# Kernel optimization log

Hardware: AMD Instinct MI355X
Metric: run time of the kernel (lower is better)

The kernel has to match this reference:

```python
import jax, jax.numpy as jnp
import numpy as np

G, N, DEG = 64, 2048, 8          # graphs, nodes/graph, avg degree
NTOT = G * N                      # 131072 nodes
E = NTOT * DEG                    # 1048576 edges
K = int(np.ceil(0.2 * N))         # 410 nodes kept per graph (SAGPooling ratio=0.2)
NK = G * K                        # 26240 pooled nodes
H, C = 3, 20                      # GAT heads, per-head channels
NEG_BIG = jnp.float32(-1e30)


def gcn(x, src, dst, W, b, n):
    """PyG GCNConv: x' = D^-1/2 (A+I) D^-1/2 x W + b (edge weight 1)."""
    h = x @ W
    deg = jax.ops.segment_sum(jnp.ones(src.shape[0], x.dtype), dst, num_segments=n) + 1.0
    dinv = jax.lax.rsqrt(deg)
    coef = dinv[src] * dinv[dst]                    # [E]
    agg = jax.ops.segment_sum(h[src] * coef[:, None], dst, num_segments=n)
    agg = agg + h * (dinv * dinv)[:, None]          # self loops
    return agg + b


def setup_inputs() -> dict:
    key = jax.random.key(0)
    ks = jax.random.split(key, 16)
    # edges constrained within each graph: per-graph local indices + offsets
    off = jnp.repeat(jnp.arange(G, dtype=jnp.int32) * N, N * DEG)   # [E]
    src = jax.random.randint(ks[0], (E,), 0, N, dtype=jnp.int32) + off
    dst = jax.random.randint(ks[1], (E,), 0, N, dtype=jnp.int32) + off
    batch = jnp.repeat(jnp.arange(G, dtype=jnp.int32), N)           # [NTOT]
    x = jax.random.normal(ks[2], (NTOT, 5), jnp.float32)
    s = 0.1
    return {
        "x": x, "src": src, "dst": dst, "batch": batch,
        "W1": jax.random.normal(ks[3], (5, 10)) * s,   "b1": jnp.zeros((10,)),
        "Ws": jax.random.normal(ks[4], (10, 1)) * s,   "bs": jnp.zeros((1,)),
        "Wg": jax.random.normal(ks[5], (10, H * C)) * s,
        "a_src": jax.random.normal(ks[6], (H, C)) * s,
        "a_dst": jax.random.normal(ks[7], (H, C)) * s,
        "bg": jnp.zeros((H * C,)),
        "Wf1": jax.random.normal(ks[8], (60, 30)) * s, "bf1": jnp.zeros((30,)),
        "Wf2": jax.random.normal(ks[9], (30, 3)) * s,  "bf2": jnp.zeros((3,)),
    }


def reference(x, src, dst, batch, W1, b1, Ws, bs, Wg, a_src, a_dst, bg, Wf1, bf1, Wf2, bf2):
    n = x.shape[0]
    # GCNConv(5,10)
    x1 = gcn(x, src, dst, W1, b1, n)                              # [NTOT,10]
    # SAGPooling: GCN scorer, top-k per graph, gate by tanh(score)
    score = gcn(x1, src, dst, Ws, bs, n)[:, 0]                    # [NTOT]
    _, topi = jax.lax.top_k(score.reshape(G, N), K)               # [G,K]
    perm = (topi + (jnp.arange(G) * N)[:, None]).reshape(-1)      # [NK] global ids
    xp = x1[perm] * jnp.tanh(score[perm])[:, None]                # [NK,10]
    # remap edges; drop (mask) edges touching removed nodes (filter_adj)
    new_idx = jnp.full((n,), -1, jnp.int32).at[perm].set(jnp.arange(NK, dtype=jnp.int32))
    s2, d2 = new_idx[src], new_idx[dst]
    emask = (s2 >= 0) & (d2 >= 0)
    s2 = jnp.where(emask, s2, 0)
    d2 = jnp.where(emask, d2, 0)
    # GATConv(10, 20, heads=3) with self loops
    h = (xp @ Wg).reshape(NK, H, C)
    al_s = jnp.sum(h * a_src, -1)                                 # [NK,H]
    al_d = jnp.sum(h * a_dst, -1)
    loop = jnp.arange(NK, dtype=jnp.int32)
    sa = jnp.concatenate([s2, loop])
    da = jnp.concatenate([d2, loop])
    ma = jnp.concatenate([emask, jnp.ones((NK,), bool)])
    logits = jax.nn.leaky_relu(al_s[sa] + al_d[da], 0.2)          # [E+NK,H]
    logits = jnp.where(ma[:, None], logits, NEG_BIG)
    mx = jax.ops.segment_max(logits, da, num_segments=NK)         # finite: self loops
    w = jnp.exp(logits - mx[da]) * ma[:, None]
    denom = jax.ops.segment_sum(w, da, num_segments=NK)
    alpha = w / denom[da]                                         # edge softmax
    out = jax.ops.segment_sum(h[sa] * alpha[..., None], da, num_segments=NK)  # [NK,H,C]
    xg = out.reshape(NK, H * C) + bg                              # concat heads -> 60
    # scatter_add readout over graphs
    g = jax.ops.segment_sum(xg, batch[perm], num_segments=G)      # [G,60]
    # MLP + LogSoftmax
    z = jax.nn.relu(g @ Wf1 + bf1) @ Wf2 + bf2                    # [G,3]
    return jax.nn.log_softmax(z, axis=1)
```

## Files before the change

### kernel.cpp

```cpp
#include <hip/hip_runtime.h>
#include <math.h>

#define G    64
#define NPG  2048
#define NTOT (G * NPG)
#define EPG  (NPG * 8)
#define KSEL 410
#define NH   3
#define NC   20
#define HC   60
#define FCAP 24
#define KPAD 512
#define RP   12

#define OFF_H1P   0
#define OFF_XP    0
#define OFF_FADJ  16400
#define OFF_FCNT  36080
#define OFF_HF    37728
#define OFF_CSR   98304
#define OFF_HIST  131072
#define OFF_RS    139264
#define OFF_ALS   139264
#define OFF_ALD   144184
#define OFF_SK    147456
#define OFF_WRED  149104
#define OFF_GOUT  151024
#define OFF_HID   151264
#define OFF_NEWL  155648
#define OFF_PERML 159744
#define OFF_WSUM  160568
#define OFF_FLAGS 160632
#define ARENA_SZ  160648

__device__ inline float leaky(float x) { return x >= 0.f ? x : 0.2f * x; }

__device__ inline int wave_incl_scan(int v) {
    int lane = threadIdx.x & 63;
#pragma unroll
    for (int d = 1; d < 64; d <<= 1) {
        int t = __shfl_up(v, d, 64);
        if (lane >= d) v += t;
    }
    return v;
}

__global__ __launch_bounds__(1024) void k_all(
    const float* __restrict__ x, const int* __restrict__ src, const int* __restrict__ dst,
    const float* __restrict__ W1, const float* __restrict__ b1,
    const float* __restrict__ Ws, const float* __restrict__ bs,
    const float* __restrict__ Wg, const float* __restrict__ a_srcw,
    const float* __restrict__ a_dstw, const float* __restrict__ bg,
    const float* __restrict__ Wf1, const float* __restrict__ bf1,
    const float* __restrict__ Wf2, const float* __restrict__ bf2,
    float* __restrict__ out)
{
    __shared__ __align__(16) char arena[ARENA_SZ];
    float*          h1p   = (float*)(arena + OFF_H1P);
    float*          xpL   = (float*)(arena + OFF_XP);
    unsigned short* fadjL = (unsigned short*)(arena + OFF_FADJ);
    int*            fcntL = (int*)(arena + OFF_FCNT);
    float*          hfL   = (float*)(arena + OFF_HF);
    unsigned short* csrL  = (unsigned short*)(arena + OFF_CSR);
    int*            hist  = (int*)(arena + OFF_HIST);
    int*            rsL   = (int*)(arena + OFF_RS);
    float*          alsL  = (float*)(arena + OFF_ALS);
    float*          aldL  = (float*)(arena + OFF_ALD);
    unsigned*       skL   = (unsigned*)(arena + OFF_SK);
    float*          wred  = (float*)(arena + OFF_WRED);
    float*          goutL = (float*)(arena + OFF_GOUT);
    float*          hidL  = (float*)(arena + OFF_HID);
    unsigned short* newLs = (unsigned short*)(arena + OFF_NEWL);
    unsigned short* permL = (unsigned short*)(arena + OFF_PERML);
    int*            wsumL = (int*)(arena + OFF_WSUM);
    int*            flags = (int*)(arena + OFF_FLAGS);
#define bselS  flags[0]
#define bneedS flags[1]
#define curS   flags[2]
#define totS   flags[3]

    int g = blockIdx.x, tid = threadIdx.x, wid = tid >> 6;
    int nbase = g * NPG, ebase = g * EPG;

    for (int i = tid; i < NPG; i += 1024) hist[i] = 0;
    for (int i = tid; i < NPG; i += 1024) {
        float xi[5];
#pragma unroll
        for (int k = 0; k < 5; k++) xi[k] = x[(size_t)(nbase + i) * 5 + k];
        float v[10];
#pragma unroll
        for (int j = 0; j < 10; j++) {
            float s = 0.f;
#pragma unroll
            for (int k = 0; k < 5; k++) s += xi[k] * W1[k * 10 + j];
            v[j] = s;
        }
        float4* row = (float4*)(h1p + i * RP);
        row[0] = make_float4(v[0], v[1], v[2], v[3]);
        row[1] = make_float4(v[4], v[5], v[6], v[7]);
        row[2] = make_float4(v[8], v[9], 0.f, 0.f);
    }
    __syncthreads();
    for (int e = tid; e < EPG; e += 1024)
        atomicAdd(&hist[dst[ebase + e] - nbase], 1);
    __syncthreads();
    {
        int b2 = tid * 2;
        int v0 = hist[b2], v1 = hist[b2 + 1];
        int s = v0 + v1;
        int incl = wave_incl_scan(s);
        if ((tid & 63) == 63) wsumL[wid] = incl;
        __syncthreads();
        if (tid == 0) {
            int a = 0;
#pragma unroll
            for (int w = 0; w < 16; w++) { int t = wsumL[w]; wsumL[w] = a; a += t; }
        }
        __syncthreads();
        int base = wsumL[wid] + incl - s;
        rsL[b2] = base;
        rsL[b2 + 1] = base + v0;
        h1p[b2 * RP + 10] = rsqrtf((float)v0 + 1.0f);
        h1p[(b2 + 1) * RP + 10] = rsqrtf((float)v1 + 1.0f);
        hist[b2] = 0; hist[b2 + 1] = 0;
    }
    __syncthreads();
    for (int e = tid; e < EPG; e += 1024) {
        int ee = ebase + e;
        int sl = src[ee] - nbase;
        int dl = dst[ee] - nbase;
        int pos = rsL[dl] + atomicAdd(&hist[dl], 1);
        csrL[pos] = (unsigned short)sl;
    }
    __syncthreads();

    {
        int i0 = tid, i1 = tid + 1024;
        int e0 = rsL[i0], e0e = rsL[i0 + 1];
        int e1 = rsL[i1], e1e = (i1 == NPG - 1) ? EPG : rsL[i1 + 1];
        float acc0[10], acc1[10];
#pragma unroll
        for (int j = 0; j < 10; j++) { acc0[j] = 0.f; acc1[j] = 0.f; }
        while (e0 < e0e || e1 < e1e) {
            if (e0 < e0e) {
                int s = csrL[e0++];
                const float4* rw = (const float4*)(h1p + s * RP);
                float4 r0 = rw[0], r1 = rw[1], r2 = rw[2];
                float dv = r2.z;
                acc0[0] += r0.x * dv; acc0[1] += r0.y * dv; acc0[2] += r0.z * dv; acc0[3] += r0.w * dv;
                acc0[4] += r1.x * dv; acc0[5] += r1.y * dv; acc0[6] += r1.z * dv; acc0[7] += r1.w * dv;
                acc0[8] += r2.x * dv; acc0[9] += r2.y * dv;
            }
            if (e1 < e1e) {
                int s = csrL[e1++];
                const float4* rw = (const float4*)(h1p + s * RP);
                float4 r0 = rw[0], r1 = rw[1], r2 = rw[2];
                float dv = r2.z;
                acc1[0] += r0.x * dv; acc1[1] += r0.y * dv; acc1[2] += r0.z * dv; acc1[3] += r0.w * dv;
                acc1[4] += r1.x * dv; acc1[5] += r1.y * dv; acc1[6] += r1.z * dv; acc1[7] += r1.w * dv;
                acc1[8] += r2.x * dv; acc1[9] += r2.y * dv;
            }
        }
        const float4* q0 = (const float4*)(h1p + i0 * RP);
        const float4* q1 = (const float4*)(h1p + i1 * RP);
        float4 s00 = q0[0], s01 = q0[1], s02 = q0[2];
        float4 s10 = q1[0], s11 = q1[1], s12 = q1[2];
        float di0 = s02.z, d20 = di0 * di0;
        float di1 = s12.z, d21 = di1 * di1;
        float b1r[10];
#pragma unroll
        for (int j = 0; j < 10; j++) b1r[j] = b1[j];
        float v0[10], v1[10];
        v0[0] = acc0[0] * di0 + s00.x * d20 + b1r[0];
        v0[1] = acc0[1] * di0 + s00.y * d20 + b1r[1];
        v0[2] = acc0[2] * di0 + s00.z * d20 + b1r[2];
        v0[3] = acc0[3] * di0 + s00.w * d20 + b1r[3];
        v0[4] = acc0[4] * di0 + s01.x * d20 + b1r[4];
        v0[5] = acc0[5] * di0 + s01.y * d20 + b1r[5];
        v0[6] = acc0[6] * di0 + s01.z * d20 + b1r[6];
        v0[7] = acc0[7] * di0 + s01.w * d20 + b1r[7];
        v0[8] = acc0[8] * di0 + s02.x * d20 + b1r[8];
        v0[9] = acc0[9] * di0 + s02.y * d20 + b1r[9];
        v1[0] = acc1[0] * di1 + s10.x * d21 + b1r[0];
        v1[1] = acc1[1] * di1 + s10.y * d21 + b1r[1];
        v1[2] = acc1[2] * di1 + s10.z * d21 + b1r[2];
        v1[3] = acc1[3] * di1 + s10.w * d21 + b1r[3];
        v1[4] = acc1[4] * di1 + s11.x * d21 + b1r[4];
        v1[5] = acc1[5] * di1 + s11.y * d21 + b1r[5];
        v1[6] = acc1[6] * di1 + s11.z * d21 + b1r[6];
        v1[7] = acc1[7] * di1 + s11.w * d21 + b1r[7];
        v1[8] = acc1[8] * di1 + s12.x * d21 + b1r[8];
        v1[9] = acc1[9] * di1 + s12.y * d21 + b1r[9];
        float hs0 = 0.f, hs1 = 0.f;
#pragma unroll
        for (int j = 0; j < 10; j++) { float w = Ws[j]; hs0 += v0[j] * w; hs1 += v1[j] * w; }
        __syncthreads();
        float4* w0 = (float4*)(h1p + i0 * RP);
        w0[0] = make_float4(v0[0], v0[1], v0[2], v0[3]);
        w0[1] = make_float4(v0[4], v0[5], v0[6], v0[7]);
        w0[2] = make_float4(v0[8], v0[9], di0, hs0);
        float4* w1 = (float4*)(h1p + i1 * RP);
        w1[0] = make_float4(v1[0], v1[1], v1[2], v1[3]);
        w1[1] = make_float4(v1[4], v1[5], v1[6], v1[7]);
        w1[2] = make_float4(v1[8], v1[9], di1, hs1);
    }
    __syncthreads();

    {
        float bsv = bs[0];
        int i0 = tid, i1 = tid + 1024;
        float2 own0 = *(const float2*)(h1p + i0 * RP + 10);
        float2 own1 = *(const float2*)(h1p + i1 * RP + 10);
        int e0 = rsL[i0], e0e = rsL[i0 + 1];
        int e1 = rsL[i1], e1e = (i1 == NPG - 1) ? EPG : rsL[i1 + 1];
        float a0 = 0.f, a1 = 0.f;
        while (e0 < e0e || e1 < e1e) {
            if (e0 < e0e) { float2 dh = *(const float2*)(h1p + csrL[e0++] * RP + 10); a0 += dh.x * dh.y; }
            if (e1 < e1e) { float2 dh = *(const float2*)(h1p + csrL[e1++] * RP + 10); a1 += dh.x * dh.y; }
        }
        float sc0 = own0.x * a0 + own0.y * own0.x * own0.x + bsv;
        float sc1 = own1.x * a1 + own1.y * own1.x * own1.x + bsv;
        unsigned u0 = __float_as_uint(sc0);
        unsigned u1 = __float_as_uint(sc1);
        skL[i0] = (u0 & 0x80000000u) ? ~u0 : (u0 | 0x80000000u);
        skL[i1] = (u1 & 0x80000000u) ? ~u1 : (u1 | 0x80000000u);
        newLs[i0] = 0xFFFFu; newLs[i1] = 0xFFFFu;
        hist[i0] = 0; hist[i1] = 0;
    }
    if (tid == 0) curS = 0;
    int need = KSEL;
    unsigned prefix = 0;
    __syncthreads();

    for (int lv = 0; lv < 3; lv++) {
        for (int i = tid; i < NPG; i += 1024) {
            unsigned k = skL[i];
            bool match; unsigned bb;
            if (lv == 0)      { match = true;                  bb = k >> 21; }
            else if (lv == 1) { match = ((k >> 21) == prefix); bb = (k >> 10) & 0x7FFu; }
            else              { match = ((k >> 10) == prefix); bb = k & 0x3FFu; }
            if (match) atomicAdd(&hist[bb], 1);
        }
        __syncthreads();
        int b2 = tid * 2;
        int v0 = hist[b2], v1 = hist[b2 + 1];
        hist[b2] = 0; hist[b2 + 1] = 0;
        int s = v0 + v1;
        int incl = wave_incl_scan(s);
        if ((tid & 63) == 63) wsumL[wid] = incl;
        __syncthreads();
        if (tid == 0) {
            int a = 0;
#pragma unroll
            for (int w = 0; w < 16; w++) { int t = wsumL[w]; wsumL[w] = a; a += t; }
            totS = a;
        }
        __syncthreads();
        int base = wsumL[wid] + incl - s;
        int tot = totS;
        { int Sb = tot - base;        int Sb1 = Sb - v0; if (Sb >= need && Sb1 < need) { bselS = b2;     bneedS = need - Sb1; } }
        { int Sb = tot - (base + v0); int Sb1 = Sb - v1; if (Sb >= need && Sb1 < need) { bselS = b2 + 1; bneedS = need - Sb1; } }
        __syncthreads();
        if (lv == 0)      prefix = (unsigned)bselS;
        else if (lv == 1) prefix = (prefix << 11) | (unsigned)bselS;
        else              prefix = (prefix << 10) | (unsigned)bselS;
        need = bneedS;
        __syncthreads();
    }
    unsigned T = prefix;
    int greaterCnt = KSEL - need;

    for (int i = tid; i < NPG; i += 1024) {
        if (skL[i] > T) {
            int p = atomicAdd(&curS, 1);
            permL[p] = (unsigned short)i;
            newLs[i] = (unsigned short)p;
        }
    }
    {
        int b2 = tid * 2;
        int lc = 0, loc2[2];
#pragma unroll
        for (int k = 0; k < 2; k++)
            if (skL[b2 + k] == T) loc2[lc++] = b2 + k;
        __syncthreads();
        int incl = wave_incl_scan(lc);
        if ((tid & 63) == 63) wsumL[wid] = incl;
        __syncthreads();
        if (tid == 0) {
            int a = 0;
#pragma unroll
            for (int w = 0; w < 16; w++) { int t = wsumL[w]; wsumL[w] = a; a += t; }
        }
        __syncthreads();
        int rank0 = wsumL[wid] + incl - lc;
        for (int j = 0; j < lc; j++) {
            int rank = rank0 + j;
            if (rank < need) {
                int p = greaterCnt + rank;
                permL[p] = (unsigned short)loc2[j];
                newLs[loc2[j]] = (unsigned short)p;
            }
        }
    }
    __syncthreads();

    {
        float4 rq0, rq1, rq2; float tt = 0.f;
        bool havep = (tid < KSEL);
        if (havep) {
            int iL = permL[tid];
            unsigned k = skL[iL];
            unsigned u = (k & 0x80000000u) ? (k & 0x7FFFFFFFu) : ~k;
            tt = tanhf(__uint_as_float(u));
            const float4* xr = (const float4*)(h1p + iL * RP);
            rq0 = xr[0]; rq1 = xr[1]; rq2 = xr[2];
        }
        __syncthreads();
        if (havep) {
            float* xp = xpL + tid * 10;
            xp[0] = rq0.x * tt; xp[1] = rq0.y * tt; xp[2] = rq0.z * tt; xp[3] = rq0.w * tt;
            xp[4] = rq1.x * tt; xp[5] = rq1.y * tt; xp[6] = rq1.z * tt; xp[7] = rq1.w * tt;
            xp[8] = rq2.x * tt; xp[9] = rq2.y * tt;
        }
    }
    __syncthreads();

    for (int p = tid; p < KSEL; p += 1024) {
        int iL = permL[p];
        int p0 = rsL[iL], p1 = (iL == NPG - 1) ? EPG : rsL[iL + 1];
        int c = 0;
        for (int e = p0; e < p1; e++) {
            unsigned short s2 = newLs[csrL[e]];
            if (s2 != 0xFFFFu && c < FCAP) fadjL[p * FCAP + c++] = s2;
        }
        fcntL[p] = c;
    }
    __syncthreads();

    for (int t = tid; t < KSEL * NH; t += 1024) {
        int p = t / NH, hh = t - p * NH;
        float xi[10];
#pragma unroll
        for (int k = 0; k < 10; k++) xi[k] = xpL[p * 10 + k];
        float v[NC];
        float as_ = 0.f, ad_ = 0.f;
#pragma unroll
        for (int c = 0; c < NC; c++) {
            int j = hh * NC + c;
            float vv = 0.f;
#pragma unroll
            for (int k = 0; k < 10; k++) vv += xi[k] * Wg[k * HC + j];
            v[c] = vv;
            as_ += vv * a_srcw[j];
            ad_ += vv * a_dstw[j];
        }
        float4* hr = (float4*)(hfL + p * HC + hh * NC);
#pragma unroll
        for (int q = 0; q < 5; q++)
            hr[q] = make_float4(v[4 * q], v[4 * q + 1], v[4 * q + 2], v[4 * q + 3]);
        alsL[p * NH + hh] = as_;
        aldL[p * NH + hh] = ad_;
    }
    __syncthreads();

    {
        float res[NC];
#pragma unroll
        for (int rnd = 0; rnd < 2; rnd++) {
            int task = rnd == 0 ? tid : 1024 + tid;
            bool on = rnd == 0 || tid < KPAD;
            int hh = task >> 9, p = task & (KPAD - 1);
            if (on) {
                if (p < KSEL) {
                    float aldp = aldL[p * NH + hh];
                    float lself = leaky(alsL[p * NH + hh] + aldp);
                    float m = lself;
                    int c = fcntL[p];
                    const unsigned short* f = fadjL + p * FCAP;
                    for (int e = 0; e < c; e++)
                        m = fmaxf(m, leaky(alsL[f[e] * NH + hh] + aldp));
                    float wself = expf(lself - m), wsum = wself;
                    const float4* hp = (const float4*)(hfL + p * HC + hh * NC);
                    float4 r0 = hp[0], r1 = hp[1], r2 = hp[2], r3 = hp[3], r4 = hp[4];
                    r0.x *= wself; r0.y *= wself; r0.z *= wself; r0.w *= wself;
                    r1.x *= wself; r1.y *= wself; r1.z *= wself; r1.w *= wself;
                    r2.x *= wself; r2.y *= wself; r2.z *= wself; r2.w *= wself;
                    r3.x *= wself; r3.y *= wself; r3.z *= wself; r3.w *= wself;
                    r4.x *= wself; r4.y *= wself; r4.z *= wself; r4.w *= wself;
                    for (int e = 0; e < c; e++) {
                        int s2 = f[e];
                        float w = expf(leaky(alsL[s2 * NH + hh] + aldp) - m);
                        wsum += w;
                        const float4* hq = (const float4*)(hfL + s2 * HC + hh * NC);
                        float4 t0 = hq[0], t1 = hq[1], t2 = hq[2], t3 = hq[3], t4 = hq[4];
                        r0.x += w * t0.x; r0.y += w * t0.y; r0.z += w * t0.z; r0.w += w * t0.w;
                        r1.x += w * t1.x; r1.y += w * t1.y; r1.z += w * t1.z; r1.w += w * t1.w;
                        r2.x += w * t2.x; r2.y += w * t2.y; r2.z += w * t2.z; r2.w += w * t2.w;
                        r3.x += w * t3.x; r3.y += w * t3.y; r3.z += w * t3.z; r3.w += w * t3.w;
                        r4.x += w * t4.x; r4.y += w * t4.y; r4.z += w * t4.z; r4.w += w * t4.w;
                    }
                    float inv = 1.f / wsum;
                    res[0] = r0.x * inv;  res[1] = r0.y * inv;  res[2] = r0.z * inv;  res[3] = r0.w * inv;
                    res[4] = r1.x * inv;  res[5] = r1.y * inv;  res[6] = r1.z * inv;  res[7] = r1.w * inv;
                    res[8] = r2.x * inv;  res[9] = r2.y * inv;  res[10] = r2.z * inv; res[11] = r2.w * inv;
                    res[12] = r3.x * inv; res[13] = r3.y * inv; res[14] = r3.z * inv; res[15] = r3.w * inv;
                    res[16] = r4.x * inv; res[17] = r4.y * inv; res[18] = r4.z * inv; res[19] = r4.w * inv;
                } else {
#pragma unroll
                    for (int cc = 0; cc < NC; cc++) res[cc] = 0.f;
                }
#pragma unroll
                for (int cc = 0; cc < NC; cc++) {
                    float v = res[cc];
#pragma unroll
                    for (int d = 1; d < 64; d <<= 1) v += __shfl_xor(v, d, 64);
                    res[cc] = v;
                }
                if ((tid & 63) == 0) {
                    int slot = rnd == 0 ? hh * 8 + (wid & 7) : 16 + wid;
#pragma unroll
                    for (int cc = 0; cc < NC; cc++) wred[slot * NC + cc] = res[cc];
                }
            }
        }
    }
    __syncthreads();
    if (tid < HC) {
        int hh = tid / NC, c = tid - hh * NC;
        float a = 0.f;
#pragma unroll
        for (int w = 0; w < 8; w++) a += wred[(hh * 8 + w) * NC + c];
        goutL[tid] = a + (float)KSEL * bg[tid];
    }
    __syncthreads();

    if (tid < 30) {
        float s = bf1[tid];
#pragma unroll
        for (int k = 0; k < HC; k++) s += goutL[k] * Wf1[k * 30 + tid];
        hidL[tid] = s > 0.f ? s : 0.f;
    }
    __syncthreads();
    if (tid == 0) {
        float z[3];
#pragma unroll
        for (int j = 0; j < 3; j++) {
            float s = bf2[j];
            for (int k = 0; k < 30; k++) s += hidL[k] * Wf2[k * 3 + j];
            z[j] = s;
        }
        float m = fmaxf(z[0], fmaxf(z[1], z[2]));
        float lse = logf(expf(z[0] - m) + expf(z[1] - m) + expf(z[2] - m)) + m;
#pragma unroll
        for (int j = 0; j < 3; j++) out[g * 3 + j] = z[j] - lse;
    }
}

extern "C" void kernel_launch(void* const* d_in, const int* in_sizes, int n_in,
                              void* d_out, int out_size, void* d_ws, size_t ws_size,
                              hipStream_t stream) {
    const float* x     = (const float*)d_in[0];
    const int*   src   = (const int*)d_in[1];
    const int*   dst   = (const int*)d_in[2];
    const float* W1    = (const float*)d_in[4];
    const float* b1    = (const float*)d_in[5];
    const float* Ws    = (const float*)d_in[6];
    const float* bs    = (const float*)d_in[7];
    const float* Wg    = (const float*)d_in[8];
    const float* a_src = (const float*)d_in[9];
    const float* a_dst = (const float*)d_in[10];
    const float* bg    = (const float*)d_in[11];
    const float* Wf1   = (const float*)d_in[12];
    const float* bf1   = (const float*)d_in[13];
    const float* Wf2   = (const float*)d_in[14];
    const float* bf2   = (const float*)d_in[15];
    float* out = (float*)d_out;
    (void)d_ws; (void)ws_size;

    k_all<<<G, 1024, 0, stream>>>(x, src, dst, W1, b1, Ws, bs, Wg, a_src, a_dst,
                                  bg, Wf1, bf1, Wf2, bf2, out);
}
```

Measured before the change: 143.7 us.

## Scan-based top-k compaction, batched adjacency gathers, single-pass GAT softmax

Replaces the atomic-counter compaction of above-threshold nodes with a packed prefix scan that ranks greater and equal keys together, which removes atomics and makes the order deterministic. Gathers adjacency remaps in batches of 8 so the loads can overlap. The GAT softmax drops the separate max pass, normalising against the self-loop logit and using fast __expf inside an unrolled loop over the capped neighbour count. Skipping the max subtraction risks overflow when a neighbour logit greatly exceeds the self logit.

```diff
diff --git a/kernel.cpp b/kernel.cpp
--- a/kernel.cpp
+++ b/kernel.cpp
@@ -76,7 +76,6 @@
     int*            flags = (int*)(arena + OFF_FLAGS);
 #define bselS  flags[0]
 #define bneedS flags[1]
-#define curS   flags[2]
 #define totS   flags[3]
 
     int g = blockIdx.x, tid = threadIdx.x, wid = tid >> 6;
@@ -227,7 +226,6 @@
         newLs[i0] = 0xFFFFu; newLs[i1] = 0xFFFFu;
         hist[i0] = 0; hist[i1] = 0;
     }
-    if (tid == 0) curS = 0;
     int need = KSEL;
     unsigned prefix = 0;
     __syncthreads();
@@ -270,21 +268,13 @@
     unsigned T = prefix;
     int greaterCnt = KSEL - need;
 
-    for (int i = tid; i < NPG; i += 1024) {
-        if (skL[i] > T) {
-            int p = atomicAdd(&curS, 1);
-            permL[p] = (unsigned short)i;
-            newLs[i] = (unsigned short)p;
-        }
-    }
     {
         int b2 = tid * 2;
-        int lc = 0, loc2[2];
-#pragma unroll
-        for (int k = 0; k < 2; k++)
-            if (skL[b2 + k] == T) loc2[lc++] = b2 + k;
-        __syncthreads();
-        int incl = wave_incl_scan(lc);
+        unsigned k0 = skL[b2], k1 = skL[b2 + 1];
+        int gt0 = k0 > T ? 1 : 0, gt1 = k1 > T ? 1 : 0;
+        int eq0 = k0 == T ? 1 : 0, eq1 = k1 == T ? 1 : 0;
+        int pack = ((gt0 + gt1) << 16) | (eq0 + eq1);
+        int incl = wave_incl_scan(pack);
         if ((tid & 63) == 63) wsumL[wid] = incl;
         __syncthreads();
         if (tid == 0) {
@@ -293,15 +283,12 @@
             for (int w = 0; w < 16; w++) { int t = wsumL[w]; wsumL[w] = a; a += t; }
         }
         __syncthreads();
-        int rank0 = wsumL[wid] + incl - lc;
-        for (int j = 0; j < lc; j++) {
-            int rank = rank0 + j;
-            if (rank < need) {
-                int p = greaterCnt + rank;
-                permL[p] = (unsigned short)loc2[j];
-                newLs[loc2[j]] = (unsigned short)p;
-            }
-        }
+        int base = wsumL[wid] + incl - pack;
+        int gb = base >> 16, eb = base & 0xFFFF;
+        if (gt0) { permL[gb] = (unsigned short)b2; newLs[b2] = (unsigned short)gb; }
+        if (gt1) { int r = gb + gt0; permL[r] = (unsigned short)(b2 + 1); newLs[b2 + 1] = (unsigned short)r; }
+        if (eq0 && eb < need) { int p = greaterCnt + eb; permL[p] = (unsigned short)b2; newLs[b2] = (unsigned short)p; }
+        if (eq1) { int r = eb + eq0; if (r < need) { int p = greaterCnt + r; permL[p] = (unsigned short)(b2 + 1); newLs[b2 + 1] = (unsigned short)p; } }
     }
     __syncthreads();
 
@@ -330,9 +317,19 @@
         int iL = permL[p];
         int p0 = rsL[iL], p1 = (iL == NPG - 1) ? EPG : rsL[iL + 1];
         int c = 0;
-        for (int e = p0; e < p1; e++) {
-            unsigned short s2 = newLs[csrL[e]];
-            if (s2 != 0xFFFFu && c < FCAP) fadjL[p * FCAP + c++] = s2;
+        int e = p0;
+        while (e < p1) {
+            int n = p1 - e; n = n > 8 ? 8 : n;
+            int b8[8];
+#pragma unroll
+            for (int j = 0; j < 8; j++) b8[j] = csrL[e + (j < n ? j : 0)];
+            unsigned short n8[8];
+#pragma unroll
+            for (int j = 0; j < 8; j++) n8[j] = newLs[b8[j]];
+#pragma unroll
+            for (int j = 0; j < 8; j++)
+                if (j < n && n8[j] != 0xFFFFu && c < FCAP) fadjL[p * FCAP + c++] = n8[j];
+            e += n;
         }
         fcntL[p] = c;
     }
@@ -375,30 +372,24 @@
                 if (p < KSEL) {
                     float aldp = aldL[p * NH + hh];
                     float lself = leaky(alsL[p * NH + hh] + aldp);
-                    float m = lself;
                     int c = fcntL[p];
-                    const unsigned short* f = fadjL + p * FCAP;
-                    for (int e = 0; e < c; e++)
-                        m = fmaxf(m, leaky(alsL[f[e] * NH + hh] + aldp));
-                    float wself = expf(lself - m), wsum = wself;
                     const float4* hp = (const float4*)(hfL + p * HC + hh * NC);
                     float4 r0 = hp[0], r1 = hp[1], r2 = hp[2], r3 = hp[3], r4 = hp[4];
-                    r0.x *= wself; r0.y *= wself; r0.z *= wself; r0.w *= wself;
-                    r1.x *= wself; r1.y *= wself; r1.z *= wself; r1.w *= wself;
-                    r2.x *= wself; r2.y *= wself; r2.z *= wself; r2.w *= wself;
-                    r3.x *= wself; r3.y *= wself; r3.z *= wself; r3.w *= wself;
-                    r4.x *= wself; r4.y *= wself; r4.z *= wself; r4.w *= wself;
-                    for (int e = 0; e < c; e++) {
-                        int s2 = f[e];
-                        float w = expf(leaky(alsL[s2 * NH + hh] + aldp) - m);
-                        wsum += w;
-                        const float4* hq = (const float4*)(hfL + s2 * HC + hh * NC);
-                        float4 t0 = hq[0], t1 = hq[1], t2 = hq[2], t3 = hq[3], t4 = hq[4];
-                        r0.x += w * t0.x; r0.y += w * t0.y; r0.z += w * t0.z; r0.w += w * t0.w;
-                        r1.x += w * t1.x; r1.y += w * t1.y; r1.z += w * t1.z; r1.w += w * t1.w;
-                        r2.x += w * t2.x; r2.y += w * t2.y; r2.z += w * t2.z; r2.w += w * t2.w;
-                        r3.x += w * t3.x; r3.y += w * t3.y; r3.z += w * t3.z; r3.w += w * t3.w;
-                        r4.x += w * t4.x; r4.y += w * t4.y; r4.z += w * t4.z; r4.w += w * t4.w;
+                    float wsum = 1.f;
+#pragma unroll
+                    for (int e = 0; e < FCAP; e++) {
+                        if (e < c) {
+                            int idx = fadjL[p * FCAP + e];
+                            float w = __expf(leaky(alsL[idx * NH + hh] + aldp) - lself);
+                            wsum += w;
+                            const float4* hq = (const float4*)(hfL + idx * HC + hh * NC);
+                            float4 t0 = hq[0], t1 = hq[1], t2 = hq[2], t3 = hq[3], t4 = hq[4];
+                            r0.x += w * t0.x; r0.y += w * t0.y; r0.z += w * t0.z; r0.w += w * t0.w;
+                            r1.x += w * t1.x; r1.y += w * t1.y; r1.z += w * t1.z; r1.w += w * t1.w;
+                            r2.x += w * t2.x; r2.y += w * t2.y; r2.z += w * t2.z; r2.w += w * t2.w;
+                            r3.x += w * t3.x; r3.y += w * t3.y; r3.z += w * t3.z; r3.w += w * t3.w;
+                            r4.x += w * t4.x; r4.y += w * t4.y; r4.z += w * t4.z; r4.w += w * t4.w;
+                        }
                     }
                     float inv = 1.f / wsum;
                     res[0] = r0.x * inv;  res[1] = r0.y * inv;  res[2] = r0.z * inv;  res[3] = r0.w * inv;
```

Result: no change. 141.4 us (-1.6%).
